# Optimization experiments

Hardware: AMD Instinct MI355X
Metric: run time of the kernel (lower is better)

Reference implementation:

```python
import jax, jax.numpy as jnp
import numpy as np

N_NODES = 50000
N_EDGES = 1250000
D = 64
EPS = 1e-07


def setup_inputs() -> dict:
    key = jax.random.key(0)
    ks = jax.random.split(key, 10)
    return {
        "node_feats": jax.random.normal(ks[0], (N_NODES, D), jnp.float32),
        "emb0": jax.random.normal(ks[1], (8, D), jnp.float32),
        "emb1": jax.random.normal(ks[2], (4, D), jnp.float32),
        "W": jax.random.normal(ks[3], (D, D), jnp.float32) / np.sqrt(D),
        "b": jnp.zeros((D,), jnp.float32),
        "beta": jnp.ones((1,), jnp.float32),
        "scale": jnp.ones((1,), jnp.float32),
        "src": jax.random.randint(ks[4], (N_EDGES,), 0, N_NODES),
        "dst": jax.random.randint(ks[5], (N_EDGES,), 0, N_NODES),
        "edge_feat0": jax.random.randint(ks[6], (N_EDGES,), 0, 8),
        "edge_feat1": jax.random.randint(ks[7], (N_EDGES,), 0, 4),
    }


def reference(node_feats, emb0, emb1, W, b, beta, scale, src, dst, edge_feat0, edge_feat1):
    n = node_feats.shape[0]
    # edge embeddings summed over categorical feature types
    e = emb0[edge_feat0] + emb1[edge_feat1]              # [E, D]
    # u_add_e then relu + eps
    m = jnp.maximum(node_feats[src] + e, 0.0) + EPS      # [E, D]
    # edge softmax over edges sharing the same destination (per feature dim)
    logits = m * beta                                    # [E, D]
    mx = jax.ops.segment_max(logits, dst, num_segments=n)
    ex = jnp.exp(logits - mx[dst])
    denom = jax.ops.segment_sum(ex, dst, num_segments=n)
    a = ex / denom[dst]                                  # [E, D]
    # scatter-sum aggregation of m * a to destination nodes
    msg = jax.ops.segment_sum(m * a, dst, num_segments=n)  # [N, D]
    # MessageNorm: L2-normalize msg, rescale by ||node_feats|| * scale
    msg_unit = msg / jnp.maximum(
        jnp.linalg.norm(msg, axis=-1, keepdims=True), 1e-12)
    feats_norm = jnp.linalg.norm(node_feats, axis=-1, keepdims=True)
    msg = msg_unit * feats_norm * scale
    # residual + single-layer MLP
    feats = node_feats + msg
    return feats @ W + b
```

## Files before the change

kernel.cpp:

```cpp
#include <hip/hip_runtime.h>

#define NN 50000
#define NE 1250000
#define DD 64
#define KR 391
#define RSH 7
#define RCAP 4096
#define RCSH 12

typedef float vf2 __attribute__((ext_vector_type(2)));


__global__ __launch_bounds__(512) void k_part(
    const int4* __restrict__ src4, const int4* __restrict__ dst4,
    const int4* __restrict__ ef04, const int4* __restrict__ ef14,
    const float* __restrict__ W, float* __restrict__ Wt,
    int* __restrict__ rcur, unsigned* __restrict__ staging)
{
    __shared__ int hist[KR], rbase[KR];
    const int t  = threadIdx.x;
    const int gb = blockIdx.x;

    for (int i = t; i < KR; i += 512) hist[i] = 0;
    if (gb == 0)
        for (int i = t; i < 4096; i += 512)
            Wt[(i & 63) * DD + (i >> 6)] = W[i];
    __syncthreads();

    unsigned pay[8];
    int rr[8], lp[8];
#pragma unroll
    for (int u = 0; u < 8; ++u) rr[u] = -1;

#pragma unroll
    for (int g = 0; g < 2; ++g) {
        const int i4 = gb * 1024 + g * 512 + t;
        if (i4 < NE / 4) {
            const int4 s  = src4[i4], d = dst4[i4];
            const int4 f0 = ef04[i4], f1 = ef14[i4];
            const int ds[4] = {d.x, d.y, d.z, d.w};
            const int ss[4] = {s.x, s.y, s.z, s.w};
            const int a0[4] = {f0.x, f0.y, f0.z, f0.w};
            const int a1[4] = {f1.x, f1.y, f1.z, f1.w};
#pragma unroll
            for (int u = 0; u < 4; ++u) {
                const int k = g * 4 + u;
                rr[k]  = ds[u] >> RSH;
                pay[k] = (unsigned)ss[u] | ((unsigned)(a1[u] * 8 + a0[u]) << 16)
                         | ((unsigned)(ds[u] & 127) << 21);
            }
        }
    }
#pragma unroll
    for (int u = 0; u < 8; ++u)
        if (rr[u] >= 0) lp[u] = atomicAdd(&hist[rr[u]], 1);
    __syncthreads();

    for (int i = t; i < KR; i += 512) {
        const int h = hist[i];
        if (h) rbase[i] = atomicAdd(&rcur[i << 4], h);
    }
    __syncthreads();

#pragma unroll
    for (int u = 0; u < 8; ++u) {
        if (rr[u] >= 0) {
            const int pos = rbase[rr[u]] + lp[u];
            if (pos < RCAP) staging[(rr[u] << RCSH) + pos] = pay[u];
        }
    }
}

__global__ __launch_bounds__(256) void k_bucket(
    const unsigned* __restrict__ staging, const int* __restrict__ rcur,
    int* __restrict__ cnt, unsigned* __restrict__ bucket)
{
    __shared__ unsigned buck[128 * DD];
    __shared__ int ldeg[128];
    const int t = threadIdx.x;
    const int r = blockIdx.x;

    if (t < 128) ldeg[t] = 0;
    __syncthreads();

    const int ne = min(rcur[r << 4], RCAP);
    for (int i = t; i < ne; i += 256) {
        const unsigned p = staging[(r << RCSH) + i];
        const int d = (p >> 21) & 127;
        const int pos = atomicAdd(&ldeg[d], 1);
        if (pos < DD) buck[(d << 6) + pos] = p & 0x1FFFFFu;
    }
    __syncthreads();

    const int base_node = r << RSH;
    const int nnodes = min(128, NN - base_node);
    for (int i = t; i < nnodes * DD; i += 256)
        bucket[((size_t)base_node << 6) + i] = buck[i];
    if (t < nnodes) cnt[base_node + t] = min(ldeg[t], DD);
}

__global__ __launch_bounds__(256, 4) void genconv_agg(
    const float* __restrict__ nf,
    const float* __restrict__ emb0, const float* __restrict__ emb1,
    const float* __restrict__ Wt,  const float* __restrict__ b,
    const float* __restrict__ beta_p, const float* __restrict__ scale_p,
    const int* __restrict__ cnt,
    float* out)
{
    __shared__ __align__(16) float emb_s[32 * DD];
    __shared__ __align__(16) float feat_s[4][DD];

    const int w    = threadIdx.x >> 6;
    const int lane = threadIdx.x & 63;
    const int hl   = lane & 31;
    const int hi   = lane >> 5;

    for (int i = threadIdx.x; i < 32 * DD; i += 256) {
        const int r = i >> 6, c = i & 63;
        emb_s[i] = emb0[(r & 7) * DD + c] + emb1[(r >> 3) * DD + c];
    }

    float4 wc[16];
#pragma unroll
    for (int k = 0; k < 16; ++k)
        wc[k] = *(const float4*)(Wt + lane * DD + 4 * k);

    const float bias  = b[lane];
    const float b2e   = beta_p[0] * 1.44269504088896f;
    const float scale = scale_p[0];
    __syncthreads();

    const vf2* __restrict__ nf2  = (const vf2*)nf;
    const vf2* __restrict__ emb2 = (const vf2*)emb_s;
    const unsigned* bucket = (const unsigned*)out;
    const int stride = gridDim.x * 4;
    const vf2 zero = {0.0f, 0.0f};

    int node = blockIdx.x * 4 + w;
    unsigned pl = bucket[(size_t)node * DD + lane];
    int cn = min(cnt[node], DD);

    while (node < NN) {
        const int nnext = node + stride;
        unsigned pl_n = 0u;
        int cn_n = 0;
        if (nnext < NN) {
            pl_n = bucket[(size_t)nnext * DD + lane];
            cn_n = cnt[nnext];
        }
        const vf2 f2 = nf2[(node << 5) + hl];

        vf2 num2 = zero, den2 = zero;

        for (int j = 0; j < cn; j += 32) {
            vf2 a2[16];
            unsigned qv[16];
#pragma unroll
            for (int u = 0; u < 16; ++u) {
                const unsigned qA =
                    (unsigned)__builtin_amdgcn_readlane((int)pl, j + 2 * u);
                const unsigned qB =
                    (unsigned)__builtin_amdgcn_readlane((int)pl, j + 2 * u + 1);
                const unsigned q = hi ? qB : qA;
                qv[u] = q;
                const int row = (j + 2 * u + hi < cn) ? (int)(q & 0xFFFFu) : 0;
                a2[u] = nf2[(row << 5) + hl];
            }
#pragma unroll
            for (int u = 0; u < 16; ++u) {
                const vf2 e2 = emb2[(((qv[u] >> 16) & 31) << 5) + hl];
                const vf2 m  = __builtin_elementwise_max(a2[u] + e2, zero);
                const vf2 bm = m * b2e;
                vf2 x;
                x.x = exp2f(bm.x);
                x.y = exp2f(bm.y);
                const bool valid = (j + 2 * u + hi) < cn;
                x.x = valid ? x.x : 0.0f;
                x.y = valid ? x.y : 0.0f;
                den2 += x;
                num2 += m * x;
            }
        }

        num2.x += __shfl_xor(num2.x, 32, 64);
        num2.y += __shfl_xor(num2.y, 32, 64);
        den2.x += __shfl_xor(den2.x, 32, 64);
        den2.y += __shfl_xor(den2.y, 32, 64);

        num2 += den2 * 1e-7f;

        vf2 msg2;
        msg2.x = (den2.x > 0.f) ? num2.x / den2.x : 0.f;
        msg2.y = (den2.y > 0.f) ? num2.y / den2.y : 0.f;

        float ss = msg2.x * msg2.x + msg2.y * msg2.y;
        float fs = f2.x * f2.x + f2.y * f2.y;
#pragma unroll
        for (int m = 16; m >= 1; m >>= 1) {
            ss += __shfl_xor(ss, m, 64);
            fs += __shfl_xor(fs, m, 64);
        }

        const float coef =
            (1.0f / fmaxf(sqrtf(ss), 1e-12f)) * sqrtf(fs) * scale;
        const vf2 feat2 = f2 + msg2 * coef;

        ((vf2*)feat_s[w])[hl] = feat2;

        float acc = bias;
#pragma unroll
        for (int k = 0; k < 16; ++k) {
            const float4 fv = *(const float4*)&feat_s[w][4 * k];
            acc = fmaf(fv.x, wc[k].x, acc);
            acc = fmaf(fv.y, wc[k].y, acc);
            acc = fmaf(fv.z, wc[k].z, acc);
            acc = fmaf(fv.w, wc[k].w, acc);
        }
        out[(size_t)node * DD + lane] = acc;

        node = nnext;
        pl = pl_n;
        cn = min(cn_n, DD);
    }
}

extern "C" void kernel_launch(void* const* d_in, const int* in_sizes, int n_in,
                              void* d_out, int out_size, void* d_ws, size_t ws_size,
                              hipStream_t stream)
{
    const float* nf    = (const float*)d_in[0];
    const float* emb0  = (const float*)d_in[1];
    const float* emb1  = (const float*)d_in[2];
    const float* W     = (const float*)d_in[3];
    const float* b     = (const float*)d_in[4];
    const float* beta  = (const float*)d_in[5];
    const float* scale = (const float*)d_in[6];
    const int* src = (const int*)d_in[7];
    const int* dst = (const int*)d_in[8];
    const int* ef0 = (const int*)d_in[9];
    const int* ef1 = (const int*)d_in[10];

    int*      rcur    = (int*)d_ws;
    int*      cnt     = rcur + KR * 16 + 16;
    float*    Wt      = (float*)(cnt + 50048);
    unsigned* staging = (unsigned*)(Wt + 4096);

    hipMemsetAsync(rcur, 0, (size_t)(KR * 16 + 16) * sizeof(int), stream);

    k_part<<<(NE / 4 + 1023) / 1024, 512, 0, stream>>>(
        (const int4*)src, (const int4*)dst, (const int4*)ef0, (const int4*)ef1,
        W, Wt, rcur, staging);

    k_bucket<<<KR, 256, 0, stream>>>(staging, rcur, cnt, (unsigned*)d_out);

    genconv_agg<<<4096, 256, 0, stream>>>(
        nf, emb0, emb1, Wt, b, beta, scale, cnt, (float*)d_out);
}
```

Measured before the change: 226.7 us.

## Gather 4 edges per wave with float4 lanes and move W to LDS

The aggregation kernel now splits each wave into four 16-lane groups, so each group gathers a different edge with 16-byte float4 loads, replacing the earlier two 32-lane groups with 8-byte loads. Full 32-edge chunks skip the per-edge validity masks, and only a separate tail chunk keeps them. The 64x64 weight matrix is now staged in shared memory in every block rather than held as 64 registers per lane, which removes the transpose step from the partition kernel. The aim is wider memory transactions and lower register pressure, at the cost of extra shared-memory reads in the matvec and a larger LDS footprint per block.

```diff
diff --git a/kernel.cpp b/kernel.cpp
--- a/kernel.cpp
+++ b/kernel.cpp
@@ -8,13 +8,12 @@
 #define RCAP 4096
 #define RCSH 12
 
-typedef float vf2 __attribute__((ext_vector_type(2)));
+typedef float vf4 __attribute__((ext_vector_type(4)));
 
 
 __global__ __launch_bounds__(512) void k_part(
     const int4* __restrict__ src4, const int4* __restrict__ dst4,
     const int4* __restrict__ ef04, const int4* __restrict__ ef14,
-    const float* __restrict__ W, float* __restrict__ Wt,
     int* __restrict__ rcur, unsigned* __restrict__ staging)
 {
     __shared__ int hist[KR], rbase[KR];
@@ -22,9 +21,6 @@
     const int gb = blockIdx.x;
 
     for (int i = t; i < KR; i += 512) hist[i] = 0;
-    if (gb == 0)
-        for (int i = t; i < 4096; i += 512)
-            Wt[(i & 63) * DD + (i >> 6)] = W[i];
     __syncthreads();
 
     unsigned pay[8];
@@ -102,39 +98,37 @@
 __global__ __launch_bounds__(256, 4) void genconv_agg(
     const float* __restrict__ nf,
     const float* __restrict__ emb0, const float* __restrict__ emb1,
-    const float* __restrict__ Wt,  const float* __restrict__ b,
+    const float* __restrict__ W,   const float* __restrict__ b,
     const float* __restrict__ beta_p, const float* __restrict__ scale_p,
     const int* __restrict__ cnt,
     float* out)
 {
     __shared__ __align__(16) float emb_s[32 * DD];
+    __shared__ __align__(16) float W_s[DD * DD];
     __shared__ __align__(16) float feat_s[4][DD];
 
     const int w    = threadIdx.x >> 6;
     const int lane = threadIdx.x & 63;
-    const int hl   = lane & 31;
-    const int hi   = lane >> 5;
+    const int hl   = lane & 15;
+    const int hi   = lane >> 4;
 
     for (int i = threadIdx.x; i < 32 * DD; i += 256) {
         const int r = i >> 6, c = i & 63;
         emb_s[i] = emb0[(r & 7) * DD + c] + emb1[(r >> 3) * DD + c];
     }
-
-    float4 wc[16];
-#pragma unroll
-    for (int k = 0; k < 16; ++k)
-        wc[k] = *(const float4*)(Wt + lane * DD + 4 * k);
+    for (int i = threadIdx.x; i < DD * DD; i += 256)
+        W_s[i] = W[i];
 
     const float bias  = b[lane];
     const float b2e   = beta_p[0] * 1.44269504088896f;
     const float scale = scale_p[0];
     __syncthreads();
 
-    const vf2* __restrict__ nf2  = (const vf2*)nf;
-    const vf2* __restrict__ emb2 = (const vf2*)emb_s;
+    const vf4* __restrict__ nf4  = (const vf4*)nf;
+    const vf4* __restrict__ emb4 = (const vf4*)emb_s;
     const unsigned* bucket = (const unsigned*)out;
     const int stride = gridDim.x * 4;
-    const vf2 zero = {0.0f, 0.0f};
+    const vf4 zero = {0.f, 0.f, 0.f, 0.f};
 
     int node = blockIdx.x * 4 + w;
     unsigned pl = bucket[(size_t)node * DD + lane];
@@ -148,73 +142,109 @@
             pl_n = bucket[(size_t)nnext * DD + lane];
             cn_n = cnt[nnext];
         }
-        const vf2 f2 = nf2[(node << 5) + hl];
-
-        vf2 num2 = zero, den2 = zero;
-
-        for (int j = 0; j < cn; j += 32) {
-            vf2 a2[16];
-            unsigned qv[16];
-#pragma unroll
-            for (int u = 0; u < 16; ++u) {
-                const unsigned qA =
-                    (unsigned)__builtin_amdgcn_readlane((int)pl, j + 2 * u);
-                const unsigned qB =
-                    (unsigned)__builtin_amdgcn_readlane((int)pl, j + 2 * u + 1);
-                const unsigned q = hi ? qB : qA;
+        const vf4 f4 = nf4[(node << 4) + hl];
+
+        vf4 num4 = zero, den4 = zero;
+
+        int j = 0;
+        for (; j + 32 <= cn; j += 32) {
+            vf4 a4[8];
+            unsigned qv[8];
+#pragma unroll
+            for (int u = 0; u < 8; ++u) {
+                const int base = j + 4 * u;
+                const unsigned q0 = (unsigned)__builtin_amdgcn_readlane((int)pl, base + 0);
+                const unsigned q1 = (unsigned)__builtin_amdgcn_readlane((int)pl, base + 1);
+                const unsigned q2 = (unsigned)__builtin_amdgcn_readlane((int)pl, base + 2);
+                const unsigned q3 = (unsigned)__builtin_amdgcn_readlane((int)pl, base + 3);
+                const unsigned s01 = (hi & 1) ? q1 : q0;
+                const unsigned s23 = (hi & 1) ? q3 : q2;
+                const unsigned q   = (hi & 2) ? s23 : s01;
                 qv[u] = q;
-                const int row = (j + 2 * u + hi < cn) ? (int)(q & 0xFFFFu) : 0;
-                a2[u] = nf2[(row << 5) + hl];
-            }
-#pragma unroll
-            for (int u = 0; u < 16; ++u) {
-                const vf2 e2 = emb2[(((qv[u] >> 16) & 31) << 5) + hl];
-                const vf2 m  = __builtin_elementwise_max(a2[u] + e2, zero);
-                const vf2 bm = m * b2e;
-                vf2 x;
-                x.x = exp2f(bm.x);
-                x.y = exp2f(bm.y);
-                const bool valid = (j + 2 * u + hi) < cn;
-                x.x = valid ? x.x : 0.0f;
-                x.y = valid ? x.y : 0.0f;
-                den2 += x;
-                num2 += m * x;
-            }
-        }
-
-        num2.x += __shfl_xor(num2.x, 32, 64);
-        num2.y += __shfl_xor(num2.y, 32, 64);
-        den2.x += __shfl_xor(den2.x, 32, 64);
-        den2.y += __shfl_xor(den2.y, 32, 64);
-
-        num2 += den2 * 1e-7f;
-
-        vf2 msg2;
-        msg2.x = (den2.x > 0.f) ? num2.x / den2.x : 0.f;
-        msg2.y = (den2.y > 0.f) ? num2.y / den2.y : 0.f;
-
-        float ss = msg2.x * msg2.x + msg2.y * msg2.y;
-        float fs = f2.x * f2.x + f2.y * f2.y;
-#pragma unroll
-        for (int m = 16; m >= 1; m >>= 1) {
+                a4[u] = nf4[((q & 0xFFFFu) << 4) + hl];
+            }
+#pragma unroll
+            for (int u = 0; u < 8; ++u) {
+                const vf4 e4 = emb4[((qv[u] >> 16) << 4) + hl];
+                const vf4 m  = __builtin_elementwise_max(a4[u] + e4, zero);
+                const vf4 bm = m * b2e;
+                vf4 x;
+                x.x = exp2f(bm.x); x.y = exp2f(bm.y);
+                x.z = exp2f(bm.z); x.w = exp2f(bm.w);
+                den4 += x;
+                num4 += m * x;
+            }
+        }
+        if (j < cn) {
+#pragma unroll
+            for (int u = 0; u < 8; ++u) {
+                const int base = j + 4 * u;
+                const unsigned q0 = (unsigned)__builtin_amdgcn_readlane((int)pl, base + 0);
+                const unsigned q1 = (unsigned)__builtin_amdgcn_readlane((int)pl, base + 1);
+                const unsigned q2 = (unsigned)__builtin_amdgcn_readlane((int)pl, base + 2);
+                const unsigned q3 = (unsigned)__builtin_amdgcn_readlane((int)pl, base + 3);
+                const unsigned s01 = (hi & 1) ? q1 : q0;
+                const unsigned s23 = (hi & 1) ? q3 : q2;
+                const unsigned q   = (hi & 2) ? s23 : s01;
+                const bool valid = (base + hi) < cn;
+                const int row = valid ? (int)(q & 0xFFFFu) : 0;
+                const vf4 a4 = nf4[(row << 4) + hl];
+                const vf4 e4 = emb4[(((q >> 16) & 31) << 4) + hl];
+                const vf4 m  = __builtin_elementwise_max(a4 + e4, zero);
+                const vf4 bm = m * b2e;
+                vf4 x;
+                x.x = valid ? exp2f(bm.x) : 0.f;
+                x.y = valid ? exp2f(bm.y) : 0.f;
+                x.z = valid ? exp2f(bm.z) : 0.f;
+                x.w = valid ? exp2f(bm.w) : 0.f;
+                den4 += x;
+                num4 += m * x;
+            }
+        }
+
+#pragma unroll
+        for (int m = 16; m <= 32; m <<= 1) {
+            num4.x += __shfl_xor(num4.x, m, 64);
+            num4.y += __shfl_xor(num4.y, m, 64);
+            num4.z += __shfl_xor(num4.z, m, 64);
+            num4.w += __shfl_xor(num4.w, m, 64);
+            den4.x += __shfl_xor(den4.x, m, 64);
+            den4.y += __shfl_xor(den4.y, m, 64);
+            den4.z += __shfl_xor(den4.z, m, 64);
+            den4.w += __shfl_xor(den4.w, m, 64);
+        }
+
+        num4 += den4 * 1e-7f;
+
+        vf4 msg4;
+        msg4.x = (den4.x > 0.f) ? num4.x / den4.x : 0.f;
+        msg4.y = (den4.y > 0.f) ? num4.y / den4.y : 0.f;
+        msg4.z = (den4.z > 0.f) ? num4.z / den4.z : 0.f;
+        msg4.w = (den4.w > 0.f) ? num4.w / den4.w : 0.f;
+
+        float ss = msg4.x * msg4.x + msg4.y * msg4.y
+                 + msg4.z * msg4.z + msg4.w * msg4.w;
+        float fs = f4.x * f4.x + f4.y * f4.y + f4.z * f4.z + f4.w * f4.w;
+#pragma unroll
+        for (int m = 8; m >= 1; m >>= 1) {
             ss += __shfl_xor(ss, m, 64);
             fs += __shfl_xor(fs, m, 64);
         }
 
         const float coef =
             (1.0f / fmaxf(sqrtf(ss), 1e-12f)) * sqrtf(fs) * scale;
-        const vf2 feat2 = f2 + msg2 * coef;
-
-        ((vf2*)feat_s[w])[hl] = feat2;
+        const vf4 feat4 = f4 + msg4 * coef;
+
+        ((vf4*)feat_s[w])[hl] = feat4;
 
         float acc = bias;
 #pragma unroll
-        for (int k = 0; k < 16; ++k) {
-            const float4 fv = *(const float4*)&feat_s[w][4 * k];
-            acc = fmaf(fv.x, wc[k].x, acc);
-            acc = fmaf(fv.y, wc[k].y, acc);
-            acc = fmaf(fv.z, wc[k].z, acc);
-            acc = fmaf(fv.w, wc[k].w, acc);
+        for (int k = 0; k < DD; k += 4) {
+            const float4 fv = *(const float4*)&feat_s[w][k];
+            acc = fmaf(fv.x, W_s[(k + 0) * DD + lane], acc);
+            acc = fmaf(fv.y, W_s[(k + 1) * DD + lane], acc);
+            acc = fmaf(fv.z, W_s[(k + 2) * DD + lane], acc);
+            acc = fmaf(fv.w, W_s[(k + 3) * DD + lane], acc);
         }
         out[(size_t)node * DD + lane] = acc;
 
@@ -242,17 +272,16 @@
 
     int*      rcur    = (int*)d_ws;
     int*      cnt     = rcur + KR * 16 + 16;
-    float*    Wt      = (float*)(cnt + 50048);
-    unsigned* staging = (unsigned*)(Wt + 4096);
+    unsigned* staging = (unsigned*)(cnt + 50048);
 
     hipMemsetAsync(rcur, 0, (size_t)(KR * 16 + 16) * sizeof(int), stream);
 
     k_part<<<(NE / 4 + 1023) / 1024, 512, 0, stream>>>(
         (const int4*)src, (const int4*)dst, (const int4*)ef0, (const int4*)ef1,
-        W, Wt, rcur, staging);
+        rcur, staging);
 
     k_bucket<<<KR, 256, 0, stream>>>(staging, rcur, cnt, (unsigned*)d_out);
 
     genconv_agg<<<4096, 256, 0, stream>>>(
-        nf, emb0, emb1, Wt, b, beta, scale, cnt, (float*)d_out);
-}
+        nf, emb0, emb1, W, b, beta, scale, cnt, (float*)d_out);
+}
```

Result: faster. 214.3 us (-5.5%).
